# Kernel optimization log

Hardware: AMD Instinct MI355X
Metric: run time of the kernel (lower is better)

## Reference

```python
import jax, jax.numpy as jnp
import numpy as np
import math

NUM_HEADS = 16
GRID_SIZE = 32
NUM_BUCKETS = 32
MAX_DISTANCE = 128
EMBED_DIM = 1024


def _rel_pos_bucket(rel, num_buckets, max_distance):
    # T5-style bucketing, as written in the source (int truncation of log branch)
    is_neg = (rel < 0).astype(jnp.int32)
    rel = jnp.abs(rel)
    rel = jnp.clip(rel, 0, max_distance - 1)
    max_exact = num_buckets // 2
    log_branch = max_exact + (
        jnp.log(rel.astype(jnp.float32) / max_exact)
        / math.log(max_distance / max_exact)
        * (num_buckets - max_exact)
    ).astype(jnp.int32)
    bucket = is_neg * num_buckets + jnp.where(rel < max_exact, rel.astype(jnp.int32), log_branch)
    return bucket  # in [0, 2*num_buckets)


def setup_inputs() -> dict:
    key = jax.random.key(0)
    ks = jax.random.split(key, 9)
    B, N, D = 4, GRID_SIZE * GRID_SIZE, EMBED_DIM
    s = 0.02
    return {
        "query": jax.random.normal(ks[0], (B, N, D), jnp.float32),
        "key": jax.random.normal(ks[1], (B, N, D), jnp.float32),
        "value": jax.random.normal(ks[2], (B, N, D), jnp.float32),
        "in_proj_w": jax.random.normal(ks[3], (3 * D, D), jnp.float32) * s,
        "in_proj_b": jnp.zeros((3 * D,), jnp.float32),
        "out_proj_w": jax.random.normal(ks[4], (D, D), jnp.float32) * s,
        "out_proj_b": jnp.zeros((D,), jnp.float32),
        "rel_bias_table": jax.random.normal(ks[5], (2 * NUM_BUCKETS, NUM_HEADS), jnp.float32) * s,
    }


def reference(query, key, value, in_proj_w, in_proj_b, out_proj_w, out_proj_b, rel_bias_table):
    B, N, D = query.shape
    H = NUM_HEADS
    hd = D // H
    scaling = hd ** -0.5

    # in_proj applied to `query` only (source ignores key/value args)
    qkv = query @ in_proj_w.T + in_proj_b          # [B, N, 3D]
    q, k, v = jnp.split(qkv, 3, axis=-1)
    q = q.reshape(B, N, H, hd).transpose(0, 2, 1, 3)  # [B, H, N, hd]
    k = k.reshape(B, N, H, hd).transpose(0, 2, 1, 3)
    v = v.reshape(B, N, H, hd).transpose(0, 2, 1, 3)

    attn = jnp.einsum("bhnd,bhmd->bhnm", q, k) * scaling  # [B, H, N, N]

    # 2D relative-position bucket bias
    idx = jnp.arange(N)
    row = idx // GRID_SIZE
    col = idx % GRID_SIZE
    row_bucket = _rel_pos_bucket(row[:, None] - row[None, :], NUM_BUCKETS, MAX_DISTANCE)
    col_bucket = _rel_pos_bucket(col[:, None] - col[None, :], NUM_BUCKETS, MAX_DISTANCE)
    bias = rel_bias_table[row_bucket] + rel_bias_table[col_bucket]  # [N, N, H]
    attn = attn + bias.transpose(2, 0, 1)[None]  # [B, H, N, N]

    attn_weights = jax.nn.softmax(attn, axis=-1)
    out = jnp.einsum("bhnm,bhmd->bhnd", attn_weights, v)  # [B, H, N, hd]
    out = out.transpose(0, 2, 1, 3).reshape(B, N, D)
    out = out @ out_proj_w.T + out_proj_b
    return out, attn_weights
```

## Files before the change

### kernel.cpp

```cpp
#include <hip/hip_runtime.h>
#include <hip/hip_bf16.h>

typedef __attribute__((ext_vector_type(8))) short bf16x8;
typedef __attribute__((ext_vector_type(4))) float f32x4;
typedef __attribute__((ext_vector_type(4))) unsigned short us4;

#define MFMA16(a,b,c) __builtin_amdgcn_mfma_f32_16x16x32_bf16((a),(b),(c),0,0,0)

__device__ __forceinline__ unsigned short f2bf(float f){
  unsigned u = __builtin_bit_cast(unsigned, f);
  u += 0x7fffu + ((u>>16)&1u);
  return (unsigned short)(u>>16);
}
__device__ __forceinline__ float bf2f(unsigned short h){
  unsigned u = ((unsigned)h)<<16;
  return __builtin_bit_cast(float, u);
}
__device__ __forceinline__ void gload_lds16(const unsigned short* g, unsigned short* l){
  __builtin_amdgcn_global_load_lds((const __attribute__((address_space(1))) void*)g,
                                   (__attribute__((address_space(3))) void*)l,
                                   16, 0, 0);
}

__global__ __launch_bounds__(256) void cast_all(
    const float* __restrict__ q, const float* __restrict__ wi, const float* __restrict__ wo,
    unsigned short* __restrict__ qq, unsigned short* __restrict__ wib, unsigned short* __restrict__ wob)
{
  int i4 = (blockIdx.x*256 + threadIdx.x)*4;
  const float* src; unsigned short* dst; int off;
  if (i4 < 4194304)       { src=q;  dst=qq;  off=i4; }
  else if (i4 < 7340032)  { src=wi; dst=wib; off=i4-4194304; }
  else                    { src=wo; dst=wob; off=i4-7340032; }
  float4 v = *(const float4*)(src+off);
  us4 o; o.x=f2bf(v.x); o.y=f2bf(v.y); o.z=f2bf(v.z); o.w=f2bf(v.w);
  *(us4*)(dst+off) = o;
}

__global__ __launch_bounds__(256) void gemm_qkv(
    const unsigned short* __restrict__ A, const unsigned short* __restrict__ Bw,
    const float* __restrict__ bias,
    unsigned short* __restrict__ qo, unsigned short* __restrict__ ko, unsigned short* __restrict__ vTo)
{
  __shared__ unsigned short lA[128*64];
  __shared__ unsigned short lB[128*64];
  int tid = threadIdx.x, lane = tid&63, w = tid>>6;
  int wr = (w>>1)<<6, wc = (w&1)<<6;
  int rowT = blockIdx.y<<7, colT = blockIdx.x<<7;
  f32x4 acc[4][4] = {};
  for (int k0=0; k0<1024; k0+=64){
    #pragma unroll
    for (int it=0; it<4; ++it){
      int ci = it*256+tid; int r=ci>>3, cs=ci&7;
      int c = (cs ^ (r&7))<<3;
      gload_lds16(A + (size_t)(rowT+r)*1024 + k0 + c, &lA[ci<<3]);
    }
    #pragma unroll
    for (int it=0; it<4; ++it){
      int ci = it*256+tid; int r=ci>>3, cs=ci&7;
      int c = (cs ^ (r&7))<<3;
      gload_lds16(Bw + (size_t)(colT+r)*1024 + k0 + c, &lB[ci<<3]);
    }
    asm volatile("s_waitcnt vmcnt(0)" ::: "memory");
    __syncthreads();
    #pragma unroll
    for (int kk=0; kk<2; ++kk){
      int kc = (kk<<2) + (lane>>4);
      bf16x8 a[4], b[4];
      #pragma unroll
      for (int i=0;i<4;++i){
        int r = wr + (i<<4) + (lane&15);
        a[i] = *(const bf16x8*)&lA[(r<<6) + ((kc ^ (r&7))<<3)];
      }
      #pragma unroll
      for (int j=0;j<4;++j){
        int r = wc + (j<<4) + (lane&15);
        b[j] = *(const bf16x8*)&lB[(r<<6) + ((kc ^ (r&7))<<3)];
      }
      #pragma unroll
      for (int i=0;i<4;++i)
        #pragma unroll
        for (int j=0;j<4;++j)
          acc[i][j] = MFMA16(a[i], b[j], acc[i][j]);
    }
    __syncthreads();
  }
  int sec = colT >> 10;
  #pragma unroll
  for (int i=0;i<4;++i){
    #pragma unroll
    for (int j=0;j<4;++j){
      int cg = colT + wc + (j<<4) + (lane&15);
      int d = cg & 1023, hh = d>>6, di = d&63;
      float bsv = bias[cg];
      #pragma unroll
      for (int q=0;q<4;++q){
        int m = rowT + wr + (i<<4) + ((lane>>4)<<2) + q;
        int b = m>>10, n = m&1023;
        unsigned short bv = f2bf(acc[i][j][q] + bsv);
        size_t bh = (size_t)((b<<4) + hh);
        if (sec==0)      qo[(bh<<16) + ((size_t)n<<6) + di] = bv;
        else if (sec==1) ko[(bh<<16) + ((size_t)n<<6) + di] = bv;
        else             vTo[(bh<<16) + ((size_t)di<<10) + n] = bv;
      }
    }
  }
}

__global__ __launch_bounds__(256) void gemm_out(
    const unsigned short* __restrict__ A, const unsigned short* __restrict__ Bw,
    const float* __restrict__ bias, float* __restrict__ out)
{
  __shared__ unsigned short lA[128*64];
  __shared__ unsigned short lB[128*64];
  int tid = threadIdx.x, lane = tid&63, w = tid>>6;
  int wr = (w>>1)<<6, wc = (w&1)<<6;
  int rowT = blockIdx.y<<7, colT = blockIdx.x<<7;
  f32x4 acc[4][4] = {};
  for (int k0=0; k0<1024; k0+=64){
    #pragma unroll
    for (int it=0; it<4; ++it){
      int ci = it*256+tid; int r=ci>>3, cs=ci&7;
      int c = (cs ^ (r&7))<<3;
      gload_lds16(A + (size_t)(rowT+r)*1024 + k0 + c, &lA[ci<<3]);
    }
    #pragma unroll
    for (int it=0; it<4; ++it){
      int ci = it*256+tid; int r=ci>>3, cs=ci&7;
      int c = (cs ^ (r&7))<<3;
      gload_lds16(Bw + (size_t)(colT+r)*1024 + k0 + c, &lB[ci<<3]);
    }
    asm volatile("s_waitcnt vmcnt(0)" ::: "memory");
    __syncthreads();
    #pragma unroll
    for (int kk=0; kk<2; ++kk){
      int kc = (kk<<2) + (lane>>4);
      bf16x8 a[4], b[4];
      #pragma unroll
      for (int i=0;i<4;++i){
        int r = wr + (i<<4) + (lane&15);
        a[i] = *(const bf16x8*)&lA[(r<<6) + ((kc ^ (r&7))<<3)];
      }
      #pragma unroll
      for (int j=0;j<4;++j){
        int r = wc + (j<<4) + (lane&15);
        b[j] = *(const bf16x8*)&lB[(r<<6) + ((kc ^ (r&7))<<3)];
      }
      #pragma unroll
      for (int i=0;i<4;++i)
        #pragma unroll
        for (int j=0;j<4;++j)
          acc[i][j] = MFMA16(a[i], b[j], acc[i][j]);
    }
    __syncthreads();
  }
  #pragma unroll
  for (int i=0;i<4;++i){
    #pragma unroll
    for (int j=0;j<4;++j){
      int cg = colT + wc + (j<<4) + (lane&15);
      float bsv = bias[cg];
      #pragma unroll
      for (int q=0;q<4;++q){
        int m = rowT + wr + (i<<4) + ((lane>>4)<<2) + q;
        out[(size_t)m*1024 + cg] = acc[i][j][q] + bsv;
      }
    }
  }
}

__global__ __launch_bounds__(256) void attn_fused(
    const unsigned short* __restrict__ qbf, const unsigned short* __restrict__ kbf,
    const unsigned short* __restrict__ vT, const float* __restrict__ tbl,
    float* __restrict__ attn_out, unsigned short* __restrict__ oa)
{
  __shared__ unsigned short P[32*1024];
  __shared__ unsigned short qs[32*64];
  __shared__ float biasv[64];
  __shared__ float rsum[4][32];
  __shared__ float rinv_s[32];

  int tid=threadIdx.x, lane=tid&63, w=tid>>6;
  int bid = blockIdx.x;
  int wgid = ((bid&7)<<8) + (bid>>3);
  int pair = wgid >> 5;
  int stripe = wgid & 31;
  int h = pair & 15;
  int bg = pair >> 4;
  int nbase = stripe<<5;
  const unsigned short* qg = qbf + ((size_t)pair<<16) + ((size_t)nbase<<6);
  const unsigned short* kg = kbf + ((size_t)pair<<16);
  const unsigned short* vg = vT  + ((size_t)pair<<16);

  if (tid < 63){
    int dd = tid - 31;
    int neg = dd<0 ? 1:0;
    int a = dd<0 ? -dd : dd;
    int bkt;
    if (a<16) bkt = a;
    else bkt = 16 + (int)(__logf((float)a*(1.f/16.f)) * (16.f/__logf(8.f)));
    bkt += neg*32;
    biasv[tid] = tbl[(bkt<<4) + h];
  }
  { int r=tid>>3, cs=tid&7;
    int c = (cs ^ (r&7))<<3;
    gload_lds16(qg + (r<<6) + c, &qs[tid<<3]); }
  asm volatile("s_waitcnt vmcnt(0)" ::: "memory");
  __syncthreads();

  int x = lane&15, g = lane>>4;
  float cterm[3][4];
  #pragma unroll
  for (int s=0;s<3;++s)
    #pragma unroll
    for (int q=0;q<4;++q)
      cterm[s][q] = biasv[(g<<2) + q - x + 31 + ((s-1)<<4)];

  bf16x8 qa[2][2];
  #pragma unroll
  for (int rt=0;rt<2;++rt){
    int r = (rt<<4) + x;
    #pragma unroll
    for (int hh=0;hh<2;++hh)
      qa[rt][hh] = *(const bf16x8*)&qs[(r<<6) + ((((hh<<2)+g) ^ (r&7))<<3)];
  }

  float rs[2][4] = {};
  int colW = w<<8;
  for (int ct2=0; ct2<8; ++ct2){
    int cbb = colW + (ct2<<5);
    float rterm = biasv[stripe - (cbb>>5) + 31];
    #pragma unroll
    for (int par=0; par<2; ++par){
      int cb = cbb + (par<<4);
      int j = cb + x;
      const unsigned short* kp = kg + ((size_t)j<<6) + (g<<3);
      bf16x8 bk0 = *(const bf16x8*)kp;
      bf16x8 bk1 = *(const bf16x8*)(kp+32);
      #pragma unroll
      for (int rt=0; rt<2; ++rt){
        f32x4 acc = {};
        acc = MFMA16(qa[rt][0], bk0, acc);
        acc = MFMA16(qa[rt][1], bk1, acc);
        #pragma unroll
        for (int q=0;q<4;++q){
          int r = (rt<<4) + (g<<2) + q;
          float lg = acc[q]*0.125f + rterm + cterm[rt+1-par][q];
          float e = __expf(lg);
          rs[rt][q] += e;
          int byteoff = (r<<11) + ((((j>>3) ^ (r&7)))<<4) + ((j&7)<<1);
          *(unsigned short*)((char*)P + byteoff) = f2bf(e);
        }
      }
    }
  }
  #pragma unroll
  for (int rt=0;rt<2;++rt){
    #pragma unroll
    for (int q=0;q<4;++q){
      float v = rs[rt][q];
      v += __shfl_xor(v,1); v += __shfl_xor(v,2); v += __shfl_xor(v,4); v += __shfl_xor(v,8);
      if (x==0) rsum[w][(rt<<4)+(g<<2)+q] = v;
    }
  }
  __syncthreads();
  if (tid<32) rinv_s[tid] = 1.f/(rsum[0][tid]+rsum[1][tid]+rsum[2][tid]+rsum[3][tid]);
  __syncthreads();

  float* ao = attn_out + ((size_t)pair<<20) + ((size_t)nbase<<10);
  for (int it=0; it<16; ++it){
    int r = (it<<1) + (tid>>7);
    int c8 = (tid&127)<<3;
    int byteoff = (r<<11) + ((((c8>>3) ^ (r&7)))<<4);
    bf16x8 pv8 = *(const bf16x8*)((char*)P + byteoff);
    float ri = rinv_s[r];
    float4 o0, o1;
    o0.x = bf2f((unsigned short)pv8[0])*ri;
    o0.y = bf2f((unsigned short)pv8[1])*ri;
    o0.z = bf2f((unsigned short)pv8[2])*ri;
    o0.w = bf2f((unsigned short)pv8[3])*ri;
    o1.x = bf2f((unsigned short)pv8[4])*ri;
    o1.y = bf2f((unsigned short)pv8[5])*ri;
    o1.z = bf2f((unsigned short)pv8[6])*ri;
    o1.w = bf2f((unsigned short)pv8[7])*ri;
    *(float4*)(ao + ((size_t)r<<10) + c8)     = o0;
    *(float4*)(ao + ((size_t)r<<10) + c8 + 4) = o1;
  }

  f32x4 oacc[2] = {};
  int dbase = w<<4;
  const unsigned short* vp = vg + ((size_t)(dbase + x)<<10) + (g<<3);
  #pragma unroll 4
  for (int kc=0; kc<1024; kc+=32){
    bf16x8 bv = *(const bf16x8*)(vp + kc);
    int ck = (kc>>3) + g;
    #pragma unroll
    for (int rt=0;rt<2;++rt){
      int r = (rt<<4) + x;
      bf16x8 a = *(const bf16x8*)((char*)P + (r<<11) + ((ck ^ (r&7))<<4));
      oacc[rt] = MFMA16(a, bv, oacc[rt]);
    }
  }
  #pragma unroll
  for (int rt=0;rt<2;++rt){
    #pragma unroll
    for (int q=0;q<4;++q){
      int r = (rt<<4) + (g<<2) + q;
      float val = oacc[rt][q]*rinv_s[r];
      oa[((size_t)((bg<<10) + nbase + r)<<10) + (h<<6) + dbase + x] = f2bf(val);
    }
  }
}

extern "C" void kernel_launch(void* const* d_in, const int* in_sizes, int n_in,
                              void* d_out, int out_size, void* d_ws, size_t ws_size,
                              hipStream_t stream)
{
  const float* query = (const float*)d_in[0];
  const float* wi  = (const float*)d_in[3];
  const float* bi  = (const float*)d_in[4];
  const float* wo  = (const float*)d_in[5];
  const float* bo  = (const float*)d_in[6];
  const float* tbl = (const float*)d_in[7];

  char* ws = (char*)d_ws;
  unsigned short* qq  = (unsigned short*)(ws);
  unsigned short* wib = (unsigned short*)(ws + 8388608);
  unsigned short* wob = (unsigned short*)(ws + 14680064);
  unsigned short* qbf = (unsigned short*)(ws + 16777216);
  unsigned short* kbf = (unsigned short*)(ws + 25165824);
  unsigned short* vTb = (unsigned short*)(ws + 33554432);
  unsigned short* oa  = (unsigned short*)(ws + 41943040);

  float* out  = (float*)d_out;
  float* attn = out + 4194304;

  cast_all<<<dim3(8192), dim3(256), 0, stream>>>(query, wi, wo, qq, wib, wob);
  gemm_qkv<<<dim3(24,32), dim3(256), 0, stream>>>(qq, wib, bi, qbf, kbf, vTb);
  attn_fused<<<dim3(2048), dim3(256), 0, stream>>>(qbf, kbf, vTb, tbl, attn, oa);
  gemm_out<<<dim3(8,32), dim3(256), 0, stream>>>(oa, wob, bo, out);
}
```

Baseline: 193.0 us.

## Use nontemporal loads/stores, prefetch K, and reorder PV before attn writeout

The cast kernel now reads through nontemporal loads. The out-projection epilogue and the large fp32 attention-weight write now use nontemporal stores to avoid polluting cache. The QK^T loop is flattened into 16 steps with software prefetch of the next K fragment into registers. The PV matmul now runs before the attention-probability writeout, so the big streaming stores no longer sit ahead of the MFMA work. The prefetch adds register pressure and may reduce occupancy.

```diff
diff --git a/kernel.cpp b/kernel.cpp
--- a/kernel.cpp
+++ b/kernel.cpp
@@ -31,7 +31,7 @@
   if (i4 < 4194304)       { src=q;  dst=qq;  off=i4; }
   else if (i4 < 7340032)  { src=wi; dst=wib; off=i4-4194304; }
   else                    { src=wo; dst=wob; off=i4-7340032; }
-  float4 v = *(const float4*)(src+off);
+  f32x4 v = __builtin_nontemporal_load((const f32x4*)(src+off));
   us4 o; o.x=f2bf(v.x); o.y=f2bf(v.y); o.z=f2bf(v.z); o.w=f2bf(v.w);
   *(us4*)(dst+off) = o;
 }
@@ -162,7 +162,7 @@
       #pragma unroll
       for (int q=0;q<4;++q){
         int m = rowT + wr + (i<<4) + ((lane>>4)<<2) + q;
-        out[(size_t)m*1024 + cg] = acc[i][j][q] + bsv;
+        __builtin_nontemporal_store(acc[i][j][q] + bsv, out + (size_t)m*1024 + cg);
       }
     }
   }
@@ -226,30 +226,34 @@
 
   float rs[2][4] = {};
   int colW = w<<8;
-  for (int ct2=0; ct2<8; ++ct2){
-    int cbb = colW + (ct2<<5);
-    float rterm = biasv[stripe - (cbb>>5) + 31];
-    #pragma unroll
-    for (int par=0; par<2; ++par){
-      int cb = cbb + (par<<4);
-      int j = cb + x;
-      const unsigned short* kp = kg + ((size_t)j<<6) + (g<<3);
-      bf16x8 bk0 = *(const bf16x8*)kp;
-      bf16x8 bk1 = *(const bf16x8*)(kp+32);
-      #pragma unroll
-      for (int rt=0; rt<2; ++rt){
-        f32x4 acc = {};
-        acc = MFMA16(qa[rt][0], bk0, acc);
-        acc = MFMA16(qa[rt][1], bk1, acc);
-        #pragma unroll
-        for (int q=0;q<4;++q){
-          int r = (rt<<4) + (g<<2) + q;
-          float lg = acc[q]*0.125f + rterm + cterm[rt+1-par][q];
-          float e = __expf(lg);
-          rs[rt][q] += e;
-          int byteoff = (r<<11) + ((((j>>3) ^ (r&7)))<<4) + ((j&7)<<1);
-          *(unsigned short*)((char*)P + byteoff) = f2bf(e);
-        }
+  const unsigned short* kbase = kg + ((size_t)x<<6) + (g<<3);
+  bf16x8 nb0 = *(const bf16x8*)(kbase + ((size_t)colW<<6));
+  bf16x8 nb1 = *(const bf16x8*)(kbase + ((size_t)colW<<6) + 32);
+  #pragma unroll 2
+  for (int t=0; t<16; ++t){
+    bf16x8 bk0 = nb0, bk1 = nb1;
+    if (t < 15){
+      const unsigned short* kp = kbase + ((size_t)(colW + ((t+1)<<4))<<6);
+      nb0 = *(const bf16x8*)kp;
+      nb1 = *(const bf16x8*)(kp+32);
+    }
+    int cb = colW + (t<<4);
+    int j = cb + x;
+    int par = t&1;
+    float rterm = biasv[stripe - (cb>>5) + 31];
+    #pragma unroll
+    for (int rt=0; rt<2; ++rt){
+      f32x4 acc = {};
+      acc = MFMA16(qa[rt][0], bk0, acc);
+      acc = MFMA16(qa[rt][1], bk1, acc);
+      #pragma unroll
+      for (int q=0;q<4;++q){
+        int r = (rt<<4) + (g<<2) + q;
+        float lg = acc[q]*0.125f + rterm + cterm[rt+1-par][q];
+        float e = __expf(lg);
+        rs[rt][q] += e;
+        int byteoff = (r<<11) + ((((j>>3) ^ (r&7)))<<4) + ((j&7)<<1);
+        *(unsigned short*)((char*)P + byteoff) = f2bf(e);
       }
     }
   }
@@ -265,6 +269,30 @@
   __syncthreads();
   if (tid<32) rinv_s[tid] = 1.f/(rsum[0][tid]+rsum[1][tid]+rsum[2][tid]+rsum[3][tid]);
   __syncthreads();
+
+  f32x4 oacc[2] = {};
+  int dbase = w<<4;
+  const unsigned short* vp = vg + ((size_t)(dbase + x)<<10) + (g<<3);
+  #pragma unroll 4
+  for (int kc=0; kc<1024; kc+=32){
+    bf16x8 bv = *(const bf16x8*)(vp + kc);
+    int ck = (kc>>3) + g;
+    #pragma unroll
+    for (int rt=0;rt<2;++rt){
+      int r = (rt<<4) + x;
+      bf16x8 a = *(const bf16x8*)((char*)P + (r<<11) + ((ck ^ (r&7))<<4));
+      oacc[rt] = MFMA16(a, bv, oacc[rt]);
+    }
+  }
+  #pragma unroll
+  for (int rt=0;rt<2;++rt){
+    #pragma unroll
+    for (int q=0;q<4;++q){
+      int r = (rt<<4) + (g<<2) + q;
+      float val = oacc[rt][q]*rinv_s[r];
+      oa[((size_t)((bg<<10) + nbase + r)<<10) + (h<<6) + dbase + x] = f2bf(val);
+    }
+  }
 
   float* ao = attn_out + ((size_t)pair<<20) + ((size_t)nbase<<10);
   for (int it=0; it<16; ++it){
@@ -273,7 +301,7 @@
     int byteoff = (r<<11) + ((((c8>>3) ^ (r&7)))<<4);
     bf16x8 pv8 = *(const bf16x8*)((char*)P + byteoff);
     float ri = rinv_s[r];
-    float4 o0, o1;
+    f32x4 o0, o1;
     o0.x = bf2f((unsigned short)pv8[0])*ri;
     o0.y = bf2f((unsigned short)pv8[1])*ri;
     o0.z = bf2f((unsigned short)pv8[2])*ri;
@@ -282,32 +310,8 @@
     o1.y = bf2f((unsigned short)pv8[5])*ri;
     o1.z = bf2f((unsigned short)pv8[6])*ri;
     o1.w = bf2f((unsigned short)pv8[7])*ri;
-    *(float4*)(ao + ((size_t)r<<10) + c8)     = o0;
-    *(float4*)(ao + ((size_t)r<<10) + c8 + 4) = o1;
-  }
-
-  f32x4 oacc[2] = {};
-  int dbase = w<<4;
-  const unsigned short* vp = vg + ((size_t)(dbase + x)<<10) + (g<<3);
-  #pragma unroll 4
-  for (int kc=0; kc<1024; kc+=32){
-    bf16x8 bv = *(const bf16x8*)(vp + kc);
-    int ck = (kc>>3) + g;
-    #pragma unroll
-    for (int rt=0;rt<2;++rt){
-      int r = (rt<<4) + x;
-      bf16x8 a = *(const bf16x8*)((char*)P + (r<<11) + ((ck ^ (r&7))<<4));
-      oacc[rt] = MFMA16(a, bv, oacc[rt]);
-    }
-  }
-  #pragma unroll
-  for (int rt=0;rt<2;++rt){
-    #pragma unroll
-    for (int q=0;q<4;++q){
-      int r = (rt<<4) + (g<<2) + q;
-      float val = oacc[rt][q]*rinv_s[r];
-      oa[((size_t)((bg<<10) + nbase + r)<<10) + (h<<6) + dbase + x] = f2bf(val);
-    }
+    __builtin_nontemporal_store(o0, (f32x4*)(ao + ((size_t)r<<10) + c8));
+    __builtin_nontemporal_store(o1, (f32x4*)(ao + ((size_t)r<<10) + c8 + 4));
   }
 }
 
```

New measurement: 221.8 us. 1.15x slower.
